# Kernel optimization log

Measured on AMD Instinct MI355X. Metric: run time of the kernel, lower is better.

## Reference

```python
import jax, jax.numpy as jnp
import numpy as np

B, S, D, O, H, E, K = 4, 1024, 1024, 1024, 2048, 8, 2
EPS = 1e-5

def _layernorm(x, g, b):
    m = jnp.mean(x, axis=-1, keepdims=True)
    v = jnp.mean(jnp.square(x - m), axis=-1, keepdims=True)
    return (x - m) * jax.lax.rsqrt(v + EPS) * g + b

def setup_inputs() -> dict:
    key = jax.random.key(0)
    ks = jax.random.split(key, 8)
    def xavier(k, shape):
        fan_out, fan_in = shape[-2], shape[-1]
        bound = float(np.sqrt(6.0 / (fan_in + fan_out)))
        return jax.random.uniform(k, shape, jnp.float32, -bound, bound)
    return {
        "x": jax.random.normal(ks[0], (B, S, D), jnp.float32),
        "ln1_g": jnp.ones((D,), jnp.float32), "ln1_b": jnp.zeros((D,), jnp.float32),
        "router_w": xavier(ks[1], (E, D)), "router_b": jnp.zeros((E,), jnp.float32),
        "sh_w1": xavier(ks[2], (H, D)), "sh_b1": jnp.zeros((H,), jnp.float32),
        "sh_w2": xavier(ks[3], (O, H)), "sh_b2": jnp.zeros((O,), jnp.float32),
        "e_w1": xavier(ks[4], (E, H, D)), "e_b1": jnp.zeros((E, H), jnp.float32),
        "e_w2": xavier(ks[5], (E, O, H)), "e_b2": jnp.zeros((E, O), jnp.float32),
        "ln2_g": jnp.ones((O,), jnp.float32), "ln2_b": jnp.zeros((O,), jnp.float32),
    }

def reference(x, ln1_g, ln1_b, router_w, router_b, sh_w1, sh_b1, sh_w2, sh_b2,
              e_w1, e_b1, e_w2, e_b2, ln2_g, ln2_b):
    # eval mode: no router noise, no aux loss
    x_norm = _layernorm(x, ln1_g, ln1_b)               # [B,S,D]
    xf = x_norm.reshape(-1, D)                          # [T,D]
    logits = xf @ router_w.T + router_b                 # [T,E]
    probs = jax.nn.softmax(logits, axis=-1)
    tk_w, tk_i = jax.lax.top_k(probs, K)                # [T,K]
    tk_w = tk_w / jnp.sum(tk_w, axis=-1, keepdims=True)
    # shared expert (exact GELU, as torch nn.GELU default)
    shared = jax.nn.gelu(xf @ sh_w1.T + sh_b1, approximate=False) @ sh_w2.T + sh_b2  # [T,O]
    # all experts densely, combined sparsely by top-k weights
    hid = jax.nn.gelu(jnp.einsum('td,ehd->teh', xf, e_w1) + e_b1, approximate=False)  # [T,E,H]
    eout = jnp.einsum('teh,eoh->teo', hid, e_w2) + e_b2                                # [T,E,O]
    comb_w = jnp.sum(jax.nn.one_hot(tk_i, E, dtype=xf.dtype) * tk_w[..., None], axis=1)  # [T,E]
    out = shared * (1.0 / (E + 1)) + jnp.einsum('te,teo->to', comb_w, eout)           # [T,O]
    out = _layernorm(out.reshape(B, S, O), ln2_g, ln2_b)
    return out
```

## Files before the change

kernel.cpp:

```cpp
#include <hip/hip_runtime.h>
#include <math.h>
#include <stdint.h>

typedef unsigned short u16;
typedef unsigned int u32;

typedef __attribute__((ext_vector_type(8))) short bf16x8;
typedef __attribute__((ext_vector_type(4))) float f32x4;

#define ASYNC_COPY16(g, l)                                                         \
  __builtin_amdgcn_global_load_lds((__attribute__((address_space(1))) const void*)(g), \
                                   (__attribute__((address_space(3))) void*)(l), 16, 0, 0)

__device__ __forceinline__ float bf2f(u16 u) {
  union { u32 i; float f; } v; v.i = ((u32)u) << 16; return v.f;
}
__device__ __forceinline__ u16 f2bf(float f) {
  union { float f; u32 i; } v; v.f = f;
  u32 r = v.i + 0x7fffu + ((v.i >> 16) & 1u);
  return (u16)(r >> 16);
}
__device__ __forceinline__ float gelu_fast(float x) {
  float t = x * x;
  float z = 1.5957691f * x * (1.0f + 0.044715f * t);
  return x / (1.0f + __expf(-z));
}

__global__ __launch_bounds__(256) void cvt_all_k(
    const float* __restrict__ s0, const float* __restrict__ s1,
    const float* __restrict__ s2, const float* __restrict__ s3,
    u16* __restrict__ dst)
{
  const int64_t i0 = (int64_t)blockIdx.x * 2048 + (int64_t)threadIdx.x * 8;
  const float* src; int64_t rel;
  if (i0 < 2097152)       { src = s0; rel = i0; }
  else if (i0 < 4194304)  { src = s1; rel = i0 - 2097152; }
  else if (i0 < 20971520) { src = s2; rel = i0 - 4194304; }
  else                    { src = s3; rel = i0 - 20971520; }
  const float4 a = *(const float4*)(src + rel);
  const float4 b = *(const float4*)(src + rel + 4);
  union { u16 h[8]; uint4 v; } o;
  o.h[0] = f2bf(a.x); o.h[1] = f2bf(a.y); o.h[2] = f2bf(a.z); o.h[3] = f2bf(a.w);
  o.h[4] = f2bf(b.x); o.h[5] = f2bf(b.y); o.h[6] = f2bf(b.z); o.h[7] = f2bf(b.w);
  *(uint4*)(dst + i0) = o.v;
}

__global__ __launch_bounds__(256) void ln_router_k(
    const float* __restrict__ x, const float* __restrict__ g, const float* __restrict__ b,
    const float* __restrict__ rw, const float* __restrict__ rb,
    u16* __restrict__ xn, int* __restrict__ tk_idx, float* __restrict__ tk_w)
{
  const int t = blockIdx.x, tid = threadIdx.x;
  __shared__ float xs[1024];
  __shared__ float red[8];
  __shared__ float logits[8];
  const int wave = tid >> 6, lane = tid & 63;

  const float4 xv = *(const float4*)(x + (size_t)t * 1024 + 4 * tid);
  float v0 = xv.x, v1 = xv.y, v2 = xv.z, v3 = xv.w;
  float s = v0 + v1 + v2 + v3;
  float q = v0 * v0 + v1 * v1 + v2 * v2 + v3 * v3;
#pragma unroll
  for (int o = 32; o > 0; o >>= 1) { s += __shfl_down(s, o, 64); q += __shfl_down(q, o, 64); }
  if (lane == 0) { red[wave] = s; red[4 + wave] = q; }
  __syncthreads();
  if (tid == 0) {
    float S = red[0] + red[1] + red[2] + red[3];
    float Q = red[4] + red[5] + red[6] + red[7];
    float mean = S * (1.0f / 1024.0f);
    float var = Q * (1.0f / 1024.0f) - mean * mean;
    red[0] = mean; red[1] = rsqrtf(var + 1e-5f);
  }
  __syncthreads();
  const float mean = red[0], rstd = red[1];
  float vv[4] = {v0, v1, v2, v3};
  union { u16 h[4]; uint2 v; } pk;
#pragma unroll
  for (int j = 0; j < 4; ++j) {
    int d = 4 * tid + j;
    float y = (vv[j] - mean) * rstd * g[d] + b[d];
    xs[d] = y;
    pk.h[j] = f2bf(y);
  }
  *(uint2*)(xn + (size_t)t * 1024 + 4 * tid) = pk.v;
  __syncthreads();
#pragma unroll
  for (int pe = 0; pe < 2; ++pe) {
    int e = wave + 4 * pe;
    const float* wrow = rw + (size_t)e * 1024;
    float acc = 0.f;
#pragma unroll
    for (int j = 0; j < 16; ++j) {
      int d = lane + 64 * j;
      acc += xs[d] * wrow[d];
    }
#pragma unroll
    for (int o = 32; o > 0; o >>= 1) acc += __shfl_down(acc, o, 64);
    if (lane == 0) logits[e] = acc + rb[e];
  }
  __syncthreads();
  if (tid == 0) {
    int i0 = 0; float l0 = logits[0];
#pragma unroll
    for (int e = 1; e < 8; ++e) if (logits[e] > l0) { l0 = logits[e]; i0 = e; }
    int i1 = -1; float l1 = -3.4e38f;
#pragma unroll
    for (int e = 0; e < 8; ++e) { if (e == i0) continue; if (logits[e] > l1) { l1 = logits[e]; i1 = e; } }
    float w0 = 1.0f / (1.0f + expf(l1 - l0));
    float w1 = 1.0f - w0;
    tk_idx[2 * t] = i0; tk_idx[2 * t + 1] = i1;
    tk_w[2 * t] = w0; tk_w[2 * t + 1] = w1;
  }
}

__device__ __forceinline__ uint4 u4_add(uint4 a, uint4 b) {
  uint4 r; r.x = a.x + b.x; r.y = a.y + b.y; r.z = a.z + b.z; r.w = a.w + b.w; return r;
}
__device__ __forceinline__ uint4 u4_sub(uint4 a, uint4 b) {
  uint4 r; r.x = a.x - b.x; r.y = a.y - b.y; r.z = a.z - b.z; r.w = a.w - b.w; return r;
}

__global__ __launch_bounds__(256) void assign_k(
    const int* __restrict__ tk_idx, const float* __restrict__ tk_w,
    int* __restrict__ offs, int* __restrict__ slot_token,
    float* __restrict__ slot_w, int* __restrict__ slot_of)
{
  const int tid = threadIdx.x, lane = tid & 63, wave = tid >> 6;
  int eidx[32];
#pragma unroll
  for (int j = 0; j < 32; ++j) eidx[j] = tk_idx[tid * 32 + j];

  uint4 p = {0u, 0u, 0u, 0u};
#pragma unroll
  for (int j = 0; j < 32; ++j) {
    int e = eidx[j];
    unsigned inc = 1u << ((e & 1) * 16);
    int c = e >> 1;
    if (c == 0) p.x += inc; else if (c == 1) p.y += inc;
    else if (c == 2) p.z += inc; else p.w += inc;
  }
  const uint4 own = p;
#pragma unroll
  for (int o = 1; o < 64; o <<= 1) {
    uint4 t;
    t.x = (u32)__shfl_up((int)p.x, o, 64);
    t.y = (u32)__shfl_up((int)p.y, o, 64);
    t.z = (u32)__shfl_up((int)p.z, o, 64);
    t.w = (u32)__shfl_up((int)p.w, o, 64);
    if (lane >= o) p = u4_add(p, t);
  }
  __shared__ uint4 wtot[4];
  __shared__ int offs_s[9];
  if (lane == 63) wtot[wave] = p;
  __syncthreads();
  uint4 wbase = {0u, 0u, 0u, 0u};
  uint4 gtot = {0u, 0u, 0u, 0u};
#pragma unroll
  for (int w2 = 0; w2 < 4; ++w2) {
    uint4 t = wtot[w2];
    if (w2 < wave) wbase = u4_add(wbase, t);
    gtot = u4_add(gtot, t);
  }
  const uint4 excl = u4_sub(p, own);
  if (tid == 0) {
    int gtots[8] = { (int)(gtot.x & 0xffff), (int)(gtot.x >> 16),
                     (int)(gtot.y & 0xffff), (int)(gtot.y >> 16),
                     (int)(gtot.z & 0xffff), (int)(gtot.z >> 16),
                     (int)(gtot.w & 0xffff), (int)(gtot.w >> 16) };
    int a = 0;
#pragma unroll
    for (int e = 0; e < 8; ++e) { offs_s[e] = a; offs[e] = a; a += gtots[e]; }
    offs_s[8] = a; offs[8] = a;
  }
  __syncthreads();
  const uint4 pre = u4_add(wbase, excl);
  int base[8];
  base[0] = offs_s[0] + (int)(pre.x & 0xffff);
  base[1] = offs_s[1] + (int)(pre.x >> 16);
  base[2] = offs_s[2] + (int)(pre.y & 0xffff);
  base[3] = offs_s[3] + (int)(pre.y >> 16);
  base[4] = offs_s[4] + (int)(pre.z & 0xffff);
  base[5] = offs_s[5] + (int)(pre.z >> 16);
  base[6] = offs_s[6] + (int)(pre.w & 0xffff);
  base[7] = offs_s[7] + (int)(pre.w >> 16);
#pragma unroll
  for (int j = 0; j < 32; ++j) {
    int idx = tid * 32 + j;
    int e = eidx[j];
    int s = base[e]++;
    slot_token[s] = idx >> 1;
    slot_w[s] = tk_w[idx];
    slot_of[idx] = s;
  }
}

template <int N, int KD, int STAGE>
__global__ __launch_bounds__(256) void gemm_fused_k(
    const u16* __restrict__ Abase, const u16* __restrict__ Bsh,
    const u16* __restrict__ Bex, const float* __restrict__ bias_sh,
    const float* __restrict__ bias_ex,
    u16* __restrict__ outH,
    const int* __restrict__ offs, const int* __restrict__ slot_token,
    const float* __restrict__ slot_w)
{
  const int tid = threadIdx.x;
  const int z = blockIdx.z;
  int off = 0, cnt = 4096, obase = 0;
  const u16* B = Bsh;
  const float* biasp = bias_sh;
  if (z > 0) {
    off = offs[z - 1]; cnt = offs[z] - off; obase = 4096 + off;
    B = Bex + (size_t)(z - 1) * N * KD;
    biasp = bias_ex + (size_t)(z - 1) * N;
  }
  const int m0 = blockIdx.y * 128;
  if (m0 >= cnt) return;
  const int n0 = blockIdx.x * 128;

  __shared__ u16 lA[2][4096];
  __shared__ u16 lB[2][4096];

  const int rS = tid >> 2;
  const int c8 = (tid & 3) * 8;

  int ra0 = m0 + rS;      if (ra0 > cnt - 1) ra0 = cnt - 1;
  int ra1 = m0 + rS + 64; if (ra1 > cnt - 1) ra1 = cnt - 1;
  size_t arow0, arow1;
  if (STAGE == 1) {
    if (z == 0) { arow0 = (size_t)ra0; arow1 = (size_t)ra1; }
    else        { arow0 = (size_t)slot_token[off + ra0]; arow1 = (size_t)slot_token[off + ra1]; }
  } else {
    if (z == 0) { arow0 = (size_t)ra0; arow1 = (size_t)ra1; }
    else        { arow0 = (size_t)(4096 + off + ra0); arow1 = (size_t)(4096 + off + ra1); }
  }
  const u16* gA0 = Abase + arow0 * KD + c8;
  const u16* gA1 = Abase + arow1 * KD + c8;
  const u16* gB0 = B + (size_t)(n0 + rS) * KD + c8;
  const u16* gB1 = B + (size_t)(n0 + rS + 64) * KD + c8;

  const int wave = tid >> 6, lane = tid & 63;
  const int wr = wave >> 1, wc = wave & 1;
  const int fr = lane & 15, fq = lane >> 4;

  f32x4 acc[4][4];
  const f32x4 zero = {0.f, 0.f, 0.f, 0.f};
#pragma unroll
  for (int i = 0; i < 4; ++i)
#pragma unroll
    for (int n = 0; n < 4; ++n) acc[i][n] = zero;

  const int NK = KD / 32;
  {
    ASYNC_COPY16(gA0, &lA[0][0] + wave * 512);
    ASYNC_COPY16(gA1, &lA[0][0] + 2048 + wave * 512);
    ASYNC_COPY16(gB0, &lB[0][0] + wave * 512);
    ASYNC_COPY16(gB1, &lB[0][0] + 2048 + wave * 512);
    gA0 += 32; gA1 += 32; gB0 += 32; gB1 += 32;
  }

  for (int kb = 0; kb < NK; ++kb) {
    const int cur = kb & 1;
    __syncthreads();
    if (kb + 1 < NK) {
      ASYNC_COPY16(gA0, &lA[cur ^ 1][0] + wave * 512);
      ASYNC_COPY16(gA1, &lA[cur ^ 1][0] + 2048 + wave * 512);
      ASYNC_COPY16(gB0, &lB[cur ^ 1][0] + wave * 512);
      ASYNC_COPY16(gB1, &lB[cur ^ 1][0] + 2048 + wave * 512);
      gA0 += 32; gA1 += 32; gB0 += 32; gB1 += 32;
    }
    const u16* rdA = &lA[cur][0] + (wr * 64 + fr) * 32 + fq * 8;
    const u16* rdB = &lB[cur][0] + (wc * 64 + fr) * 32 + fq * 8;
    bf16x8 af[4], bfv[4];
#pragma unroll
    for (int i = 0; i < 4; ++i) af[i] = *(const bf16x8*)(rdA + i * 16 * 32);
#pragma unroll
    for (int n = 0; n < 4; ++n) bfv[n] = *(const bf16x8*)(rdB + n * 16 * 32);
#pragma unroll
    for (int i = 0; i < 4; ++i)
#pragma unroll
      for (int n = 0; n < 4; ++n)
        acc[i][n] = __builtin_amdgcn_mfma_f32_16x16x32_bf16(af[i], bfv[n], acc[i][n], 0, 0, 0);
  }

  const int colBase = n0 + wc * 64;
#pragma unroll
  for (int i = 0; i < 4; ++i) {
    const int mlBase = m0 + wr * 64 + i * 16 + fq * 4;
#pragma unroll
    for (int r = 0; r < 4; ++r) {
      const int ml = mlBase + r;
      if (ml >= cnt) continue;
      const size_t orow = (size_t)(obase + ml) * N;
      float rwgt = (STAGE == 2) ? ((z == 0) ? (1.0f / 9.0f) : slot_w[off + ml]) : 1.f;
#pragma unroll
      for (int n = 0; n < 4; ++n) {
        const int col = colBase + n * 16 + fr;
        float v = acc[i][n][r] + biasp[col];
        if (STAGE == 1) v = gelu_fast(v);
        else            v = v * rwgt;
        outH[orow + col] = f2bf(v);
      }
    }
  }
}

__global__ __launch_bounds__(256) void combine_ln2_k(
    const u16* __restrict__ sh_out, const u16* __restrict__ eout,
    const int* __restrict__ slot_of,
    const float* __restrict__ g2, const float* __restrict__ b2,
    float* __restrict__ out)
{
  const int t = blockIdx.x, tid = threadIdx.x;
  const int wave = tid >> 6, lane = tid & 63;
  __shared__ float red[8];
  const size_t s0 = (size_t)slot_of[2 * t], s1 = (size_t)slot_of[2 * t + 1];
  union { uint2 v; u16 h[4]; } a, c0, c1;
  a.v  = *(const uint2*)(sh_out + (size_t)t * 1024 + 4 * tid);
  c0.v = *(const uint2*)(eout + s0 * 1024 + 4 * tid);
  c1.v = *(const uint2*)(eout + s1 * 1024 + 4 * tid);
  float vv[4];
#pragma unroll
  for (int j = 0; j < 4; ++j) vv[j] = bf2f(a.h[j]) + bf2f(c0.h[j]) + bf2f(c1.h[j]);
  float s = vv[0] + vv[1] + vv[2] + vv[3];
  float q = vv[0] * vv[0] + vv[1] * vv[1] + vv[2] * vv[2] + vv[3] * vv[3];
#pragma unroll
  for (int o = 32; o > 0; o >>= 1) { s += __shfl_down(s, o, 64); q += __shfl_down(q, o, 64); }
  if (lane == 0) { red[wave] = s; red[4 + wave] = q; }
  __syncthreads();
  if (tid == 0) {
    float S = red[0] + red[1] + red[2] + red[3];
    float Q = red[4] + red[5] + red[6] + red[7];
    float mean = S * (1.0f / 1024.0f);
    float var = Q * (1.0f / 1024.0f) - mean * mean;
    red[0] = mean; red[1] = rsqrtf(var + 1e-5f);
  }
  __syncthreads();
  const float mean = red[0], rstd = red[1];
#pragma unroll
  for (int j = 0; j < 4; ++j) {
    int d = 4 * tid + j;
    out[(size_t)t * 1024 + d] = (vv[j] - mean) * rstd * g2[d] + b2[d];
  }
}

extern "C" void kernel_launch(void* const* d_in, const int* in_sizes, int n_in,
                              void* d_out, int out_size, void* d_ws, size_t ws_size,
                              hipStream_t stream)
{
  const float* x     = (const float*)d_in[0];
  const float* ln1_g = (const float*)d_in[1];
  const float* ln1_b = (const float*)d_in[2];
  const float* rw    = (const float*)d_in[3];
  const float* rb    = (const float*)d_in[4];
  const float* sh_w1 = (const float*)d_in[5];
  const float* sh_b1 = (const float*)d_in[6];
  const float* sh_w2 = (const float*)d_in[7];
  const float* sh_b2 = (const float*)d_in[8];
  const float* e_w1  = (const float*)d_in[9];
  const float* e_b1  = (const float*)d_in[10];
  const float* e_w2  = (const float*)d_in[11];
  const float* e_b2  = (const float*)d_in[12];
  const float* ln2_g = (const float*)d_in[13];
  const float* ln2_b = (const float*)d_in[14];
  float* out = (float*)d_out;

  char* w = (char*)d_ws;
  u16*   x_norm = (u16*)(w + 0);
  u16*   hid    = (u16*)(w + (8u << 20));
  u16*   outb   = (u16*)(w + (56u << 20));
  u16*   w1b    = (u16*)(w + (104u << 20));
  u16*   w2b    = (u16*)(w + (108u << 20));
  u16*   ew1b   = (u16*)(w + (112u << 20));
  u16*   ew2b   = (u16*)(w + (144u << 20));
  char*  meta   = w + (176u << 20);
  int*   tk_idx     = (int*)(meta);
  float* tk_w       = (float*)(meta + (32u << 10));
  int*   slot_token = (int*)(meta + (64u << 10));
  float* slot_w     = (float*)(meta + (96u << 10));
  int*   slot_of    = (int*)(meta + (128u << 10));
  int*   offs       = (int*)(meta + (160u << 10));

  cvt_all_k<<<18432, 256, 0, stream>>>(sh_w1, sh_w2, e_w1, e_w2, w1b);

  ln_router_k<<<4096, 256, 0, stream>>>(x, ln1_g, ln1_b, rw, rb, x_norm, tk_idx, tk_w);
  assign_k<<<1, 256, 0, stream>>>(tk_idx, tk_w, offs, slot_token, slot_w, slot_of);

  gemm_fused_k<2048, 1024, 1><<<dim3(16, 32, 9), 256, 0, stream>>>(
      x_norm, w1b, ew1b, sh_b1, e_b1, hid, offs, slot_token, nullptr);
  gemm_fused_k<1024, 2048, 2><<<dim3(8, 32, 9), 256, 0, stream>>>(
      hid, w2b, ew2b, sh_b2, e_b2, outb, offs, slot_token, slot_w);

  combine_ln2_k<<<4096, 256, 0, stream>>>(outb, outb + (size_t)4096 * 1024,
                                          slot_of, ln2_g, ln2_b, out);
}
```

Measured before the change: 439.4 us.

## Triple-buffer GEMM LDS tiles with XOR swizzle and manual waitcnt pipelining

Turns the double-buffered async global-to-LDS loads into a three-stage ring, so tile loads are issued two iterations ahead, with an explicit vmcnt wait before a raw barrier. The column chunk of each 16-byte row segment is XOR-swizzled on both the load and read sides to cut LDS bank conflicts. MFMA sections are wrapped in s_setprio. This uses more LDS per block, which may lower occupancy, and relies on hand-written waitcnt counts being correct.

```diff
diff --git a/kernel.cpp b/kernel.cpp
--- a/kernel.cpp
+++ b/kernel.cpp
@@ -217,11 +217,11 @@
   if (m0 >= cnt) return;
   const int n0 = blockIdx.x * 128;
 
-  __shared__ u16 lA[2][4096];
-  __shared__ u16 lB[2][4096];
+  __shared__ u16 lA[3][4096];
+  __shared__ u16 lB[3][4096];
 
   const int rS = tid >> 2;
-  const int c8 = (tid & 3) * 8;
+  const int c8 = (((tid & 3) ^ ((tid >> 2) & 3) ^ ((tid >> 4) & 3))) * 8;
 
   int ra0 = m0 + rS;      if (ra0 > cnt - 1) ra0 = cnt - 1;
   int ra1 = m0 + rS + 64; if (ra1 > cnt - 1) ra1 = cnt - 1;
@@ -241,6 +241,7 @@
   const int wave = tid >> 6, lane = tid & 63;
   const int wr = wave >> 1, wc = wave & 1;
   const int fr = lane & 15, fq = lane >> 4;
+  const int sg = (fq ^ (fr & 3) ^ (fr >> 2)) * 8;
 
   f32x4 acc[4][4];
   const f32x4 zero = {0.f, 0.f, 0.f, 0.f};
@@ -250,36 +251,57 @@
     for (int n = 0; n < 4; ++n) acc[i][n] = zero;
 
   const int NK = KD / 32;
+
   {
     ASYNC_COPY16(gA0, &lA[0][0] + wave * 512);
     ASYNC_COPY16(gA1, &lA[0][0] + 2048 + wave * 512);
     ASYNC_COPY16(gB0, &lB[0][0] + wave * 512);
     ASYNC_COPY16(gB1, &lB[0][0] + 2048 + wave * 512);
     gA0 += 32; gA1 += 32; gB0 += 32; gB1 += 32;
-  }
-
+    ASYNC_COPY16(gA0, &lA[1][0] + wave * 512);
+    ASYNC_COPY16(gA1, &lA[1][0] + 2048 + wave * 512);
+    ASYNC_COPY16(gB0, &lB[1][0] + wave * 512);
+    ASYNC_COPY16(gB1, &lB[1][0] + 2048 + wave * 512);
+    gA0 += 32; gA1 += 32; gB0 += 32; gB1 += 32;
+  }
+
+  int cur = 0;
   for (int kb = 0; kb < NK; ++kb) {
-    const int cur = kb & 1;
-    __syncthreads();
     if (kb + 1 < NK) {
-      ASYNC_COPY16(gA0, &lA[cur ^ 1][0] + wave * 512);
-      ASYNC_COPY16(gA1, &lA[cur ^ 1][0] + 2048 + wave * 512);
-      ASYNC_COPY16(gB0, &lB[cur ^ 1][0] + wave * 512);
-      ASYNC_COPY16(gB1, &lB[cur ^ 1][0] + 2048 + wave * 512);
+      asm volatile("s_waitcnt vmcnt(4) lgkmcnt(0)" ::: "memory");
+    } else {
+      asm volatile("s_waitcnt vmcnt(0) lgkmcnt(0)" ::: "memory");
+    }
+    __builtin_amdgcn_s_barrier();
+    __builtin_amdgcn_sched_barrier(0);
+
+    if (kb + 2 < NK) {
+      const int nx = (cur + 2 >= 3) ? cur - 1 : cur + 2;
+      u16* sA = &lA[nx][0] + wave * 512;
+      u16* sB = &lB[nx][0] + wave * 512;
+      ASYNC_COPY16(gA0, sA);
+      ASYNC_COPY16(gA1, sA + 2048);
+      ASYNC_COPY16(gB0, sB);
+      ASYNC_COPY16(gB1, sB + 2048);
       gA0 += 32; gA1 += 32; gB0 += 32; gB1 += 32;
     }
-    const u16* rdA = &lA[cur][0] + (wr * 64 + fr) * 32 + fq * 8;
-    const u16* rdB = &lB[cur][0] + (wc * 64 + fr) * 32 + fq * 8;
+
+    const u16* rdA = &lA[cur][0] + (wr * 64 + fr) * 32 + sg;
+    const u16* rdB = &lB[cur][0] + (wc * 64 + fr) * 32 + sg;
     bf16x8 af[4], bfv[4];
 #pragma unroll
     for (int i = 0; i < 4; ++i) af[i] = *(const bf16x8*)(rdA + i * 16 * 32);
 #pragma unroll
     for (int n = 0; n < 4; ++n) bfv[n] = *(const bf16x8*)(rdB + n * 16 * 32);
+    __builtin_amdgcn_s_setprio(1);
 #pragma unroll
     for (int i = 0; i < 4; ++i)
 #pragma unroll
       for (int n = 0; n < 4; ++n)
         acc[i][n] = __builtin_amdgcn_mfma_f32_16x16x32_bf16(af[i], bfv[n], acc[i][n], 0, 0, 0);
+    __builtin_amdgcn_s_setprio(0);
+
+    cur = (cur == 2) ? 0 : cur + 1;
   }
 
   const int colBase = n0 + wc * 64;
```

Result: faster. 430.2 us (-2.1%).

## Replace MoE GEMMs with 256x256 8-wave kernel using swizzled LDS and staged pipelining

Applied to the files above, without the earlier changes.

The grouped GEMM kernel changes from 128x128 tiles with 4 waves and BK=32 to 256x256 tiles with 8 waves and BK=64. It uses an XOR-swizzled LDS layout, a double-buffered 128KB LDS, and interleaved half-tile loads between MFMA phases with setprio and explicit waitcnt/barriers. The goal is more data reuse per global load, fewer bank conflicts and better overlap of loads with MFMA. In exchange it needs much more LDS and registers. The larger M tile also wastes more work on partially filled expert row blocks, since grid.y stays 32 while m0 now steps by 256.

```diff
diff --git a/kernel.cpp b/kernel.cpp
--- a/kernel.cpp
+++ b/kernel.cpp
@@ -194,8 +194,26 @@
   }
 }
 
+#define STAGE_A(h, d)                                                              \
+  { ASYNC_COPY16(pA[h][0], lds + (d) * 16384 + (h) * 8192 + w * 1024);             \
+    ASYNC_COPY16(pA[h][1], lds + (d) * 16384 + (h) * 8192 + w * 1024 + 512);       \
+    pA[h][0] += 64; pA[h][1] += 64; }
+#define STAGE_B(h, d)                                                              \
+  { ASYNC_COPY16(pB[h][0], lds + 32768 + (d) * 16384 + (h) * 8192 + w * 1024);     \
+    ASYNC_COPY16(pB[h][1], lds + 32768 + (d) * 16384 + (h) * 8192 + w * 1024 + 512); \
+    pB[h][0] += 64; pB[h][1] += 64; }
+#define LGKM0_FENCE()                                           \
+  asm volatile("s_waitcnt lgkmcnt(0)" ::: "memory");            \
+  __builtin_amdgcn_sched_barrier(0)
+#define MFMA16(Q, BV)                                                              \
+  _Pragma("unroll") for (int mi = 0; mi < 4; ++mi)                                 \
+  _Pragma("unroll") for (int ni = 0; ni < 2; ++ni) {                               \
+    Q[mi][ni] = __builtin_amdgcn_mfma_f32_16x16x32_bf16(af[mi][0], BV[ni][0], Q[mi][ni], 0, 0, 0); \
+    Q[mi][ni] = __builtin_amdgcn_mfma_f32_16x16x32_bf16(af[mi][1], BV[ni][1], Q[mi][ni], 0, 0, 0); \
+  }
+
 template <int N, int KD, int STAGE>
-__global__ __launch_bounds__(256) void gemm_fused_k(
+__global__ __launch_bounds__(512, 2) void gemm8_k(
     const u16* __restrict__ Abase, const u16* __restrict__ Bsh,
     const u16* __restrict__ Bex, const float* __restrict__ bias_sh,
     const float* __restrict__ bias_ex,
@@ -213,95 +231,138 @@
     B = Bex + (size_t)(z - 1) * N * KD;
     biasp = bias_ex + (size_t)(z - 1) * N;
   }
-  const int m0 = blockIdx.y * 128;
+  const int m0 = blockIdx.y * 256;
   if (m0 >= cnt) return;
-  const int n0 = blockIdx.x * 128;
-
-  __shared__ u16 lA[2][4096];
-  __shared__ u16 lB[2][4096];
-
-  const int rS = tid >> 2;
-  const int c8 = (tid & 3) * 8;
-
-  int ra0 = m0 + rS;      if (ra0 > cnt - 1) ra0 = cnt - 1;
-  int ra1 = m0 + rS + 64; if (ra1 > cnt - 1) ra1 = cnt - 1;
-  size_t arow0, arow1;
-  if (STAGE == 1) {
-    if (z == 0) { arow0 = (size_t)ra0; arow1 = (size_t)ra1; }
-    else        { arow0 = (size_t)slot_token[off + ra0]; arow1 = (size_t)slot_token[off + ra1]; }
-  } else {
-    if (z == 0) { arow0 = (size_t)ra0; arow1 = (size_t)ra1; }
-    else        { arow0 = (size_t)(4096 + off + ra0); arow1 = (size_t)(4096 + off + ra1); }
-  }
-  const u16* gA0 = Abase + arow0 * KD + c8;
-  const u16* gA1 = Abase + arow1 * KD + c8;
-  const u16* gB0 = B + (size_t)(n0 + rS) * KD + c8;
-  const u16* gB1 = B + (size_t)(n0 + rS + 64) * KD + c8;
-
-  const int wave = tid >> 6, lane = tid & 63;
-  const int wr = wave >> 1, wc = wave & 1;
-  const int fr = lane & 15, fq = lane >> 4;
-
-  f32x4 acc[4][4];
+  const int n0 = blockIdx.x * 256;
+
+  __shared__ u16 lds[65536];
+
+  const int w = tid >> 6, l = tid & 63;
+  const int srow = w * 16 + (l >> 3);
+  const int gg8  = ((l & 7) ^ (l >> 3)) * 8;
+
+  const u16* pA[2][2];
+  const u16* pB[2][2];
+#pragma unroll
+  for (int h = 0; h < 2; ++h)
+#pragma unroll
+    for (int jj = 0; jj < 2; ++jj) {
+      int r = m0 + h * 128 + srow + jj * 8;
+      if (r > cnt - 1) r = cnt - 1;
+      size_t arow;
+      if (STAGE == 1) arow = (z == 0) ? (size_t)r : (size_t)slot_token[off + r];
+      else            arow = (z == 0) ? (size_t)r : (size_t)(4096 + off + r);
+      pA[h][jj] = Abase + arow * KD + gg8;
+      pB[h][jj] = B + (size_t)(n0 + h * 128 + srow + jj * 8) * KD + gg8;
+    }
+
+  const int wsr = w >> 2, wsc = w & 3;
+  const int fr = l & 15, fq = l >> 4;
+  const int sw0 = ((fq ^ (fr & 7))) * 8;
+  const int sw1 = (((4 | fq) ^ (fr & 7))) * 8;
+  const int aro = (wsr * 64 + fr) * 64;
+  const int bro = (wsc * 32 + fr) * 64;
+
+  f32x4 acc[2][2][4][2];
   const f32x4 zero = {0.f, 0.f, 0.f, 0.f};
 #pragma unroll
-  for (int i = 0; i < 4; ++i)
-#pragma unroll
-    for (int n = 0; n < 4; ++n) acc[i][n] = zero;
-
-  const int NK = KD / 32;
-  {
-    ASYNC_COPY16(gA0, &lA[0][0] + wave * 512);
-    ASYNC_COPY16(gA1, &lA[0][0] + 2048 + wave * 512);
-    ASYNC_COPY16(gB0, &lB[0][0] + wave * 512);
-    ASYNC_COPY16(gB1, &lB[0][0] + 2048 + wave * 512);
-    gA0 += 32; gA1 += 32; gB0 += 32; gB1 += 32;
-  }
-
-  for (int kb = 0; kb < NK; ++kb) {
-    const int cur = kb & 1;
-    __syncthreads();
-    if (kb + 1 < NK) {
-      ASYNC_COPY16(gA0, &lA[cur ^ 1][0] + wave * 512);
-      ASYNC_COPY16(gA1, &lA[cur ^ 1][0] + 2048 + wave * 512);
-      ASYNC_COPY16(gB0, &lB[cur ^ 1][0] + wave * 512);
-      ASYNC_COPY16(gB1, &lB[cur ^ 1][0] + 2048 + wave * 512);
-      gA0 += 32; gA1 += 32; gB0 += 32; gB1 += 32;
-    }
-    const u16* rdA = &lA[cur][0] + (wr * 64 + fr) * 32 + fq * 8;
-    const u16* rdB = &lB[cur][0] + (wc * 64 + fr) * 32 + fq * 8;
-    bf16x8 af[4], bfv[4];
-#pragma unroll
-    for (int i = 0; i < 4; ++i) af[i] = *(const bf16x8*)(rdA + i * 16 * 32);
-#pragma unroll
-    for (int n = 0; n < 4; ++n) bfv[n] = *(const bf16x8*)(rdB + n * 16 * 32);
-#pragma unroll
-    for (int i = 0; i < 4; ++i)
-#pragma unroll
-      for (int n = 0; n < 4; ++n)
-        acc[i][n] = __builtin_amdgcn_mfma_f32_16x16x32_bf16(af[i], bfv[n], acc[i][n], 0, 0, 0);
-  }
-
-  const int colBase = n0 + wc * 64;
-#pragma unroll
-  for (int i = 0; i < 4; ++i) {
-    const int mlBase = m0 + wr * 64 + i * 16 + fq * 4;
-#pragma unroll
-    for (int r = 0; r < 4; ++r) {
-      const int ml = mlBase + r;
-      if (ml >= cnt) continue;
-      const size_t orow = (size_t)(obase + ml) * N;
-      float rwgt = (STAGE == 2) ? ((z == 0) ? (1.0f / 9.0f) : slot_w[off + ml]) : 1.f;
-#pragma unroll
-      for (int n = 0; n < 4; ++n) {
-        const int col = colBase + n * 16 + fr;
-        float v = acc[i][n][r] + biasp[col];
-        if (STAGE == 1) v = gelu_fast(v);
-        else            v = v * rwgt;
-        outH[orow + col] = f2bf(v);
+  for (int mh = 0; mh < 2; ++mh)
+#pragma unroll
+    for (int nh = 0; nh < 2; ++nh)
+#pragma unroll
+      for (int mi = 0; mi < 4; ++mi)
+#pragma unroll
+        for (int ni = 0; ni < 2; ++ni) acc[mh][nh][mi][ni] = zero;
+
+  const int NT = KD / 64;
+
+  STAGE_A(0, 0); STAGE_B(0, 0); STAGE_A(1, 0); STAGE_B(1, 0);
+  STAGE_A(0, 1); STAGE_B(0, 1);
+  asm volatile("s_waitcnt vmcnt(4)" ::: "memory");
+  __builtin_amdgcn_s_barrier();
+
+  bf16x8 af[4][2], b0v[2][2], b1v[2][2];
+
+  for (int t = 0; t < NT; ++t) {
+    const int d = t & 1;
+    const u16* sA = lds + d * 16384;
+    const u16* sB = lds + 32768 + d * 16384;
+
+#pragma unroll
+    for (int mi = 0; mi < 4; ++mi) {
+      af[mi][0] = *(const bf16x8*)(sA + aro + mi * 1024 + sw0);
+      af[mi][1] = *(const bf16x8*)(sA + aro + mi * 1024 + sw1);
+    }
+#pragma unroll
+    for (int ni = 0; ni < 2; ++ni) {
+      b0v[ni][0] = *(const bf16x8*)(sB + bro + ni * 1024 + sw0);
+      b0v[ni][1] = *(const bf16x8*)(sB + bro + ni * 1024 + sw1);
+    }
+    if (t + 1 < NT) { STAGE_A(1, (t + 1) & 1); }
+    __builtin_amdgcn_s_barrier();
+    LGKM0_FENCE();
+    __builtin_amdgcn_s_setprio(1);
+    MFMA16(acc[0][0], b0v);
+    __builtin_amdgcn_s_setprio(0);
+    __builtin_amdgcn_s_barrier();
+
+#pragma unroll
+    for (int ni = 0; ni < 2; ++ni) {
+      b1v[ni][0] = *(const bf16x8*)(sB + 8192 + bro + ni * 1024 + sw0);
+      b1v[ni][1] = *(const bf16x8*)(sB + 8192 + bro + ni * 1024 + sw1);
+    }
+    if (t + 1 < NT) { STAGE_B(1, (t + 1) & 1); }
+    __builtin_amdgcn_s_barrier();
+    LGKM0_FENCE();
+    __builtin_amdgcn_s_setprio(1);
+    MFMA16(acc[0][1], b1v);
+    __builtin_amdgcn_s_setprio(0);
+    __builtin_amdgcn_s_barrier();
+
+#pragma unroll
+    for (int mi = 0; mi < 4; ++mi) {
+      af[mi][0] = *(const bf16x8*)(sA + 8192 + aro + mi * 1024 + sw0);
+      af[mi][1] = *(const bf16x8*)(sA + 8192 + aro + mi * 1024 + sw1);
+    }
+    if (t + 2 < NT) { STAGE_A(0, d); }
+    __builtin_amdgcn_s_barrier();
+    LGKM0_FENCE();
+    __builtin_amdgcn_s_setprio(1);
+    MFMA16(acc[1][0], b0v);
+    __builtin_amdgcn_s_setprio(0);
+    __builtin_amdgcn_s_barrier();
+
+    if (t + 2 < NT) { STAGE_B(0, d); }
+    __builtin_amdgcn_s_barrier();
+    __builtin_amdgcn_s_setprio(1);
+    MFMA16(acc[1][1], b1v);
+    __builtin_amdgcn_s_setprio(0);
+    if (t + 2 < NT)      { asm volatile("s_waitcnt vmcnt(4)" ::: "memory"); }
+    else if (t + 1 < NT) { asm volatile("s_waitcnt vmcnt(0)" ::: "memory"); }
+    __builtin_amdgcn_s_barrier();
+  }
+
+#pragma unroll
+  for (int mh = 0; mh < 2; ++mh)
+#pragma unroll
+    for (int mi = 0; mi < 4; ++mi)
+#pragma unroll
+      for (int r = 0; r < 4; ++r) {
+        const int ml = m0 + mh * 128 + wsr * 64 + mi * 16 + fq * 4 + r;
+        if (ml >= cnt) continue;
+        const size_t orow = (size_t)(obase + ml) * N;
+        float rwgt = (STAGE == 2) ? ((z == 0) ? (1.0f / 9.0f) : slot_w[off + ml]) : 1.f;
+#pragma unroll
+        for (int nh = 0; nh < 2; ++nh)
+#pragma unroll
+          for (int ni = 0; ni < 2; ++ni) {
+            const int col = n0 + nh * 128 + wsc * 32 + ni * 16 + fr;
+            float v = acc[mh][nh][mi][ni][r] + biasp[col];
+            if (STAGE == 1) v = gelu_fast(v);
+            else            v = v * rwgt;
+            outH[orow + col] = f2bf(v);
+          }
       }
-    }
-  }
 }
 
 __global__ __launch_bounds__(256) void combine_ln2_k(
@@ -385,9 +446,9 @@
   ln_router_k<<<4096, 256, 0, stream>>>(x, ln1_g, ln1_b, rw, rb, x_norm, tk_idx, tk_w);
   assign_k<<<1, 256, 0, stream>>>(tk_idx, tk_w, offs, slot_token, slot_w, slot_of);
 
-  gemm_fused_k<2048, 1024, 1><<<dim3(16, 32, 9), 256, 0, stream>>>(
+  gemm8_k<2048, 1024, 1><<<dim3(8, 32, 9), 512, 0, stream>>>(
       x_norm, w1b, ew1b, sh_b1, e_b1, hid, offs, slot_token, nullptr);
-  gemm_fused_k<1024, 2048, 2><<<dim3(8, 32, 9), 256, 0, stream>>>(
+  gemm8_k<1024, 2048, 2><<<dim3(4, 32, 9), 512, 0, stream>>>(
       hid, w2b, ew2b, sh_b2, e_b2, outb, offs, slot_token, slot_w);
 
   combine_ln2_k<<<4096, 256, 0, stream>>>(outb, outb + (size_t)4096 * 1024,
```

Measured after the change: 453.6 us. +3.2%, slower.

## Enlarge GEMM tiles to 256x256 with 512 threads and swizzled LDS layout

Applied to the files above, without the earlier changes.

Both grouped GEMM kernels move from 128x128 tiles and 4 waves to 256x256 tiles with 8 waves. Each wave now computes a 128x64 sub-tile, and global-to-LDS staging uses an XOR swizzle on the 16-byte column groups to cut LDS bank conflicts on the fragment reads. The larger tiles raise reuse of A and B data per load, which lowers global traffic. In exchange, per-expert row padding wastes more work, the grid has fewer blocks (occupancy and load balance may suffer), and register pressure rises from 32 accumulators per thread.

```diff
diff --git a/kernel.cpp b/kernel.cpp
--- a/kernel.cpp
+++ b/kernel.cpp
@@ -195,7 +195,7 @@
 }
 
 template <int N, int KD, int STAGE>
-__global__ __launch_bounds__(256) void gemm_fused_k(
+__global__ __launch_bounds__(512) void gemm2_k(
     const u16* __restrict__ Abase, const u16* __restrict__ Bsh,
     const u16* __restrict__ Bex, const float* __restrict__ bias_sh,
     const float* __restrict__ bias_ex,
@@ -213,18 +213,19 @@
     B = Bex + (size_t)(z - 1) * N * KD;
     biasp = bias_ex + (size_t)(z - 1) * N;
   }
-  const int m0 = blockIdx.y * 128;
+  const int m0 = blockIdx.y * 256;
   if (m0 >= cnt) return;
-  const int n0 = blockIdx.x * 128;
-
-  __shared__ u16 lA[2][4096];
-  __shared__ u16 lB[2][4096];
-
-  const int rS = tid >> 2;
-  const int c8 = (tid & 3) * 8;
-
-  int ra0 = m0 + rS;      if (ra0 > cnt - 1) ra0 = cnt - 1;
-  int ra1 = m0 + rS + 64; if (ra1 > cnt - 1) ra1 = cnt - 1;
+  const int n0 = blockIdx.x * 256;
+
+  __shared__ u16 lds[32768];
+
+  const int w = tid >> 6, l = tid & 63;
+
+  const int srow = tid >> 2;
+  const int lg   = (tid & 3) ^ ((tid >> 3) & 3);
+
+  int ra0 = m0 + srow;       if (ra0 > cnt - 1) ra0 = cnt - 1;
+  int ra1 = m0 + srow + 128; if (ra1 > cnt - 1) ra1 = cnt - 1;
   size_t arow0, arow1;
   if (STAGE == 1) {
     if (z == 0) { arow0 = (size_t)ra0; arow1 = (size_t)ra1; }
@@ -233,59 +234,58 @@
     if (z == 0) { arow0 = (size_t)ra0; arow1 = (size_t)ra1; }
     else        { arow0 = (size_t)(4096 + off + ra0); arow1 = (size_t)(4096 + off + ra1); }
   }
-  const u16* gA0 = Abase + arow0 * KD + c8;
-  const u16* gA1 = Abase + arow1 * KD + c8;
-  const u16* gB0 = B + (size_t)(n0 + rS) * KD + c8;
-  const u16* gB1 = B + (size_t)(n0 + rS + 64) * KD + c8;
-
-  const int wave = tid >> 6, lane = tid & 63;
-  const int wr = wave >> 1, wc = wave & 1;
-  const int fr = lane & 15, fq = lane >> 4;
-
-  f32x4 acc[4][4];
+  const u16* gA0 = Abase + arow0 * KD + lg * 8;
+  const u16* gA1 = Abase + arow1 * KD + lg * 8;
+  const u16* gB0 = B + (size_t)(n0 + srow) * KD + lg * 8;
+  const u16* gB1 = B + (size_t)(n0 + srow + 128) * KD + lg * 8;
+
+  const int wm = w >> 2, wn = w & 3;
+  const int fr = l & 15, fq = l >> 4;
+  const int pg = (fq ^ ((fr >> 1) & 3)) * 8;
+  const int arBase = (wm * 128 + fr) * 32 + pg;
+  const int brBase = 8192 + (wn * 64 + fr) * 32 + pg;
+
+  f32x4 acc[8][4];
   const f32x4 zero = {0.f, 0.f, 0.f, 0.f};
 #pragma unroll
-  for (int i = 0; i < 4; ++i)
-#pragma unroll
-    for (int n = 0; n < 4; ++n) acc[i][n] = zero;
-
-  const int NK = KD / 32;
-  {
-    ASYNC_COPY16(gA0, &lA[0][0] + wave * 512);
-    ASYNC_COPY16(gA1, &lA[0][0] + 2048 + wave * 512);
-    ASYNC_COPY16(gB0, &lB[0][0] + wave * 512);
-    ASYNC_COPY16(gB1, &lB[0][0] + 2048 + wave * 512);
-    gA0 += 32; gA1 += 32; gB0 += 32; gB1 += 32;
-  }
-
-  for (int kb = 0; kb < NK; ++kb) {
+  for (int mi = 0; mi < 8; ++mi)
+#pragma unroll
+    for (int ni = 0; ni < 4; ++ni) acc[mi][ni] = zero;
+
+  const int NT = KD / 32;
+
+#define STAGE_TILE(d)                                             \
+  { u16* sbA = lds + (d) * 16384 + w * 512;                       \
+    u16* sbB = lds + (d) * 16384 + 8192 + w * 512;                \
+    ASYNC_COPY16(gA0, sbA);                                       \
+    ASYNC_COPY16(gA1, sbA + 4096);                                \
+    ASYNC_COPY16(gB0, sbB);                                       \
+    ASYNC_COPY16(gB1, sbB + 4096);                                \
+    gA0 += 32; gA1 += 32; gB0 += 32; gB1 += 32; }
+
+  STAGE_TILE(0);
+
+  for (int kb = 0; kb < NT; ++kb) {
     const int cur = kb & 1;
     __syncthreads();
-    if (kb + 1 < NK) {
-      ASYNC_COPY16(gA0, &lA[cur ^ 1][0] + wave * 512);
-      ASYNC_COPY16(gA1, &lA[cur ^ 1][0] + 2048 + wave * 512);
-      ASYNC_COPY16(gB0, &lB[cur ^ 1][0] + wave * 512);
-      ASYNC_COPY16(gB1, &lB[cur ^ 1][0] + 2048 + wave * 512);
-      gA0 += 32; gA1 += 32; gB0 += 32; gB1 += 32;
-    }
-    const u16* rdA = &lA[cur][0] + (wr * 64 + fr) * 32 + fq * 8;
-    const u16* rdB = &lB[cur][0] + (wc * 64 + fr) * 32 + fq * 8;
-    bf16x8 af[4], bfv[4];
-#pragma unroll
-    for (int i = 0; i < 4; ++i) af[i] = *(const bf16x8*)(rdA + i * 16 * 32);
-#pragma unroll
-    for (int n = 0; n < 4; ++n) bfv[n] = *(const bf16x8*)(rdB + n * 16 * 32);
-#pragma unroll
-    for (int i = 0; i < 4; ++i)
-#pragma unroll
-      for (int n = 0; n < 4; ++n)
-        acc[i][n] = __builtin_amdgcn_mfma_f32_16x16x32_bf16(af[i], bfv[n], acc[i][n], 0, 0, 0);
-  }
-
-  const int colBase = n0 + wc * 64;
-#pragma unroll
-  for (int i = 0; i < 4; ++i) {
-    const int mlBase = m0 + wr * 64 + i * 16 + fq * 4;
+    if (kb + 1 < NT) { STAGE_TILE(cur ^ 1); }
+
+    const u16* sA = lds + cur * 16384;
+    bf16x8 af[8], bv[4];
+#pragma unroll
+    for (int mi = 0; mi < 8; ++mi) af[mi] = *(const bf16x8*)(sA + arBase + mi * 512);
+#pragma unroll
+    for (int ni = 0; ni < 4; ++ni) bv[ni] = *(const bf16x8*)(sA + brBase + ni * 512);
+#pragma unroll
+    for (int mi = 0; mi < 8; ++mi)
+#pragma unroll
+      for (int ni = 0; ni < 4; ++ni)
+        acc[mi][ni] = __builtin_amdgcn_mfma_f32_16x16x32_bf16(af[mi], bv[ni], acc[mi][ni], 0, 0, 0);
+  }
+
+#pragma unroll
+  for (int mi = 0; mi < 8; ++mi) {
+    const int mlBase = m0 + wm * 128 + mi * 16 + fq * 4;
 #pragma unroll
     for (int r = 0; r < 4; ++r) {
       const int ml = mlBase + r;
@@ -293,15 +293,16 @@
       const size_t orow = (size_t)(obase + ml) * N;
       float rwgt = (STAGE == 2) ? ((z == 0) ? (1.0f / 9.0f) : slot_w[off + ml]) : 1.f;
 #pragma unroll
-      for (int n = 0; n < 4; ++n) {
-        const int col = colBase + n * 16 + fr;
-        float v = acc[i][n][r] + biasp[col];
+      for (int ni = 0; ni < 4; ++ni) {
+        const int col = n0 + wn * 64 + ni * 16 + fr;
+        float v = acc[mi][ni][r] + biasp[col];
         if (STAGE == 1) v = gelu_fast(v);
         else            v = v * rwgt;
         outH[orow + col] = f2bf(v);
       }
     }
   }
+#undef STAGE_TILE
 }
 
 __global__ __launch_bounds__(256) void combine_ln2_k(
@@ -385,9 +386,9 @@
   ln_router_k<<<4096, 256, 0, stream>>>(x, ln1_g, ln1_b, rw, rb, x_norm, tk_idx, tk_w);
   assign_k<<<1, 256, 0, stream>>>(tk_idx, tk_w, offs, slot_token, slot_w, slot_of);
 
-  gemm_fused_k<2048, 1024, 1><<<dim3(16, 32, 9), 256, 0, stream>>>(
+  gemm2_k<2048, 1024, 1><<<dim3(8, 16, 9), 512, 0, stream>>>(
       x_norm, w1b, ew1b, sh_b1, e_b1, hid, offs, slot_token, nullptr);
-  gemm_fused_k<1024, 2048, 2><<<dim3(8, 32, 9), 256, 0, stream>>>(
+  gemm2_k<1024, 2048, 2><<<dim3(4, 16, 9), 512, 0, stream>>>(
       hid, w2b, ew2b, sh_b2, e_b2, outb, offs, slot_token, slot_w);
 
   combine_ln2_k<<<4096, 256, 0, stream>>>(outb, outb + (size_t)4096 * 1024,
```

Result: slower. 454.3 us (+3.4%).
